# Optimization experiments

Hardware: AMD Instinct MI355X
Metric: run time of the kernel (lower is better)

## Reference

```python
import jax, jax.numpy as jnp
import numpy as np

S, B, D = 2048, 2, 1024
NH, DH, DI = 16, 64, 4096


def setup_inputs() -> dict:
    key = jax.random.key(0)
    ks = jax.random.split(key, 12)
    init_qkv = 1.0 / np.sqrt(D)
    init_out = 1.0 / np.sqrt(NH * DH)
    stdm = 1.0 / np.sqrt(D)
    stdi = 1.0 / np.sqrt(DI)

    def u(k, shape, lo, hi):
        return jax.random.uniform(k, shape, jnp.float32, lo, hi)

    inp = {}
    inp["dec_inp"] = jax.random.normal(ks[0], (S, B, D), jnp.float32)
    # causal mask: True = masked (future key j > query i); shape [q, k, batch]
    causal = jnp.triu(jnp.ones((S, S), bool), k=1)
    inp["attn_mask"] = jnp.broadcast_to(causal[:, :, None], (S, S, B))
    inp["query_mean"] = u(ks[1], (NH * DH, D), -init_qkv, init_qkv)
    inp["key_mean"] = u(ks[2], (NH * DH, D), -init_qkv, init_qkv)
    inp["value_mean"] = u(ks[3], (NH * DH, D), -init_qkv, init_qkv)
    inp["query_std"] = u(ks[4], (NH * DH, D), 2 * np.log(init_qkv), np.log(init_qkv))
    inp["key_std"] = u(ks[5], (NH * DH, D), 2 * np.log(init_qkv), np.log(init_qkv))
    inp["value_std"] = u(ks[6], (NH * DH, D), 2 * np.log(init_qkv), np.log(init_qkv))
    inp["output_mean"] = u(ks[7], (D, NH * DH), -init_out, init_out)
    inp["output_std"] = u(ks[8], (D, NH * DH), 2 * np.log(init_out), np.log(init_out))
    inp["ln1_gamma"] = jnp.ones((D,), jnp.float32)
    inp["ln1_beta"] = jnp.zeros((D,), jnp.float32)
    inp["w1_mean"] = u(ks[9], (DI, D), -stdm, stdm)
    inp["w2_mean"] = u(ks[10], (D, DI), -stdi, stdi)
    inp["w1_std"] = u(ks[11], (DI, D), 2 * np.log(stdm), np.log(stdm))
    inp["w2_std"] = u(jax.random.fold_in(key, 99), (D, DI), 2 * np.log(stdi), np.log(stdi))
    inp["ln2_gamma"] = jnp.ones((D,), jnp.float32)
    inp["ln2_beta"] = jnp.zeros((D,), jnp.float32)
    return inp


def _layer_norm(x, g, b, eps=1e-5):
    mu = jnp.mean(x, -1, keepdims=True)
    var = jnp.mean((x - mu) ** 2, -1, keepdims=True)
    return g * (x - mu) * jax.lax.rsqrt(var + eps) + b


def _kl(theta_mean, theta_std):
    return jnp.mean(theta_mean ** 2 - 2.0 * theta_std + jnp.exp(2.0 * theta_std)) / 2.0


def reference(dec_inp, attn_mask, query_mean, key_mean, value_mean, query_std,
              key_std, value_std, output_mean, output_std, ln1_gamma, ln1_beta,
              w1_mean, w2_mean, w1_std, w2_std, ln2_gamma, ln2_beta):
    scale = 1.0 / (DH ** 0.5)
    # QKV projections (eval mode: no Bayesian weight sampling, diffs are 0)
    head_q = jnp.einsum('ibd,hd->ibh', dec_inp, query_mean).reshape(S, B, NH, DH)
    head_k = jnp.einsum('ibd,hd->ibh', dec_inp, key_mean).reshape(S, B, NH, DH)
    head_v = jnp.einsum('ibd,hd->ibh', dec_inp, value_mean).reshape(S, B, NH, DH)
    attn_score = jnp.einsum('ibnd,jbnd->ijbn', head_q, head_k) * scale
    attn_score = jnp.where(attn_mask[:, :, :, None], -jnp.inf, attn_score)
    attn_prob = jax.nn.softmax(attn_score, axis=1)  # softmax over key dim j
    attn_vec = jnp.einsum('ijbn,jbnd->ibnd', attn_prob, head_v).reshape(S, B, NH * DH)
    # NOTE: the original code (bug-faithfully) projects with value_mean, not output_mean
    attn_out = jnp.einsum('ibh,dh->ibd', attn_vec, value_mean)
    h = _layer_norm(dec_inp + attn_out, ln1_gamma, ln1_beta)
    attn_kl = _kl(
        jnp.concatenate([query_mean, key_mean, value_mean, output_mean.T], -1),
        jnp.concatenate([query_std, key_std, value_std, output_std.T], -1))
    # Bayesian positionwise FF (no activation in BayesPositionwiseFF)
    l1 = jnp.einsum('ibd,fd->ibf', h, w1_mean)
    l2 = jnp.einsum('ibf,df->ibd', l1, w2_mean)
    out = _layer_norm(h + l2, ln2_gamma, ln2_beta)
    ff_kl = _kl(jnp.concatenate([w1_mean, w2_mean.T], -1),
                jnp.concatenate([w1_std, w2_std.T], -1))
    return out, attn_kl + ff_kl
```

## Files before the change

kernel.cpp:

```cpp
#include <hip/hip_runtime.h>

#define S_LEN  2048
#define BATCH  2
#define DMODEL 1024
#define NHEADS 16
#define DHEAD  64
#define DFF    4096
#define MROWS  (S_LEN*BATCH)
#define QKVN   3072

typedef __attribute__((ext_vector_type(8))) short bf16x8;
typedef __attribute__((ext_vector_type(4))) float f32x4;
typedef __attribute__((ext_vector_type(4))) short s16x4;

#define NEG_BIG (-3.0e38f)
#define SCALE_LOG2 (0.125f * 1.4426950408889634f)

__device__ __forceinline__ short f2bf(float f){
  unsigned u = __float_as_uint(f);
  u += 0x7fffu + ((u >> 16) & 1u);
  return (short)(u >> 16);
}

__device__ __forceinline__ void gload16(const void* gptr, void* lptr){
  __builtin_amdgcn_global_load_lds(
      (const __attribute__((address_space(1))) unsigned int*)gptr,
      (__attribute__((address_space(3))) unsigned int*)lptr,
      16, 0, 0);
}

__global__ __launch_bounds__(256) void cast_kernel(const float* __restrict__ in,
                                                   short* __restrict__ out, int n){
  int i = (blockIdx.x * 256 + threadIdx.x) * 4;
  if (i >= n) return;
  f32x4 v = *(const f32x4*)(in + i);
  s16x4 o;
  o[0] = f2bf(v[0]); o[1] = f2bf(v[1]); o[2] = f2bf(v[2]); o[3] = f2bf(v[3]);
  *(s16x4*)(out + i) = o;
}

template<int BN>
__global__ __launch_bounds__(512) void gemm_bt(const short* __restrict__ A,
                                               const short* __restrict__ Bt,
                                               float* __restrict__ Cf,
                                               short* __restrict__ Cb,
                                               int M, int N, int K){
  __shared__ short As[128][32];
  __shared__ short Bs[BN][32];
  constexpr int NB = BN / 32;
  const int t = threadIdx.x;
  const int lane = t & 63, w = t >> 6;
  const int m0 = blockIdx.y * 128, n0 = blockIdx.x * BN;
  const int wm = (w & 3) * 32, wn = (w >> 2) * (BN / 2);
  const int lr = lane & 15, lg = lane >> 4;

  f32x4 acc[2][NB] = {};

  const short* Ap = A  + (size_t)(m0 + (t >> 2)) * K + (t & 3) * 8;
  const short* Bp = Bt + (size_t)(n0 + ((t & (BN * 4 - 1)) >> 2)) * K + (t & 3) * 8;
  char* ldsA = (char*)(&As[0][0]) + w * 1024;
  char* ldsB = (char*)(&Bs[0][0]) + (w & (BN / 32 * 2 - 1)) * 1024;

  for (int k0 = 0; k0 < K; k0 += 32){
    gload16(Ap + k0, ldsA);
    if (BN == 128 || t < 256) gload16(Bp + k0, ldsB);
    __syncthreads();
    bf16x8 a0 = *(const bf16x8*)&As[wm      + lr][lg * 8];
    bf16x8 a1 = *(const bf16x8*)&As[wm + 16 + lr][lg * 8];
    bf16x8 bfr[NB];
    for (int ni = 0; ni < NB; ni++)
      bfr[ni] = *(const bf16x8*)&Bs[wn + ni * 16 + lr][lg * 8];
    for (int ni = 0; ni < NB; ni++){
      acc[0][ni] = __builtin_amdgcn_mfma_f32_16x16x32_bf16(a0, bfr[ni], acc[0][ni], 0, 0, 0);
      acc[1][ni] = __builtin_amdgcn_mfma_f32_16x16x32_bf16(a1, bfr[ni], acc[1][ni], 0, 0, 0);
    }
    __syncthreads();
  }

  for (int mi = 0; mi < 2; mi++){
    for (int ni = 0; ni < NB; ni++){
      int row = m0 + wm + mi * 16 + lg * 4;
      int col = n0 + wn + ni * 16 + lr;
      for (int r = 0; r < 4; r++){
        float v = acc[mi][ni][r];
        if (Cf) Cf[(size_t)(row + r) * N + col] = v;
        if (Cb) Cb[(size_t)(row + r) * N + col] = f2bf(v);
      }
    }
  }
}

__global__ __launch_bounds__(256) void attn_kernel(const short* __restrict__ QKV,
                                                   short* __restrict__ AV){
  __shared__ short Ks[64][64];
  __shared__ short Vst[64][64];
  __shared__ short Pt[4][16][64];
  const int t = threadIdx.x, lane = t & 63, w = t >> 6;
  const int hb = blockIdx.y;
  const int b = hb >> 4, n = hb & 15;
  const int lr = lane & 15, lg = lane >> 4;

  for (int half = 0; half < 2; half++){
    const int qt = half ? (31 - (int)blockIdx.x) : (int)blockIdx.x;
    const int q0w = qt * 64 + w * 16;

    bf16x8 aq[2];
    {
      const short* qp = QKV + ((size_t)(q0w + lr) * BATCH + b) * QKVN + n * DHEAD + lg * 8;
      aq[0] = *(const bf16x8*)(qp);
      aq[1] = *(const bf16x8*)(qp + 32);
    }

    f32x4 acc[4] = {};
    float m_run = NEG_BIG, l_run = 0.f;

    for (int jt = 0; jt <= qt; jt++){
      const int j0 = jt * 64;
      __syncthreads();
      {
        int j = t >> 2, u0 = (t & 3) * 2;
        const short* kp = QKV + ((size_t)(j0 + j) * BATCH + b) * QKVN + DMODEL + n * DHEAD + u0 * 8;
        *(bf16x8*)&Ks[j][(u0 ^ (j & 7)) * 8]       = *(const bf16x8*)(kp);
        *(bf16x8*)&Ks[j][((u0 + 1) ^ (j & 7)) * 8] = *(const bf16x8*)(kp + 8);
        int jv = t & 63, dq = (t >> 6) * 16;
        const short* vp = QKV + ((size_t)(j0 + jv) * BATCH + b) * QKVN + 2 * DMODEL + n * DHEAD + dq;
        bf16x8 v0 = *(const bf16x8*)(vp);
        bf16x8 v1 = *(const bf16x8*)(vp + 8);
        int uj = jv >> 3, jl = jv & 7;
        for (int e = 0; e < 8; e++){
          int sc = (((uj ^ e) << 3) | jl);
          Vst[dq + e][sc]     = v0[e];
          Vst[dq + 8 + e][sc] = v1[e];
        }
      }
      __syncthreads();

      f32x4 s[4];
      __builtin_amdgcn_s_setprio(1);
      for (int nf = 0; nf < 4; nf++){
        f32x4 z = {};
        for (int kk = 0; kk < 2; kk++){
          bf16x8 bk = *(const bf16x8*)&Ks[nf * 16 + lr][((kk * 4 + lg) ^ (lr & 7)) * 8];
          z = __builtin_amdgcn_mfma_f32_16x16x32_bf16(bk, aq[kk], z, 0, 0, 0);
        }
        s[nf] = z;
      }
      __builtin_amdgcn_s_setprio(0);

      for (int nf = 0; nf < 4; nf++)
        for (int r = 0; r < 4; r++) s[nf][r] *= SCALE_LOG2;

      if (jt == qt){
        int qg = q0w + lr;
        for (int nf = 0; nf < 4; nf++)
          for (int r = 0; r < 4; r++)
            if (j0 + nf * 16 + lg * 4 + r > qg) s[nf][r] = NEG_BIG;
      }

      float mx = NEG_BIG;
      for (int nf = 0; nf < 4; nf++){
        float a0 = fmaxf(s[nf][0], s[nf][1]);
        float a1 = fmaxf(s[nf][2], s[nf][3]);
        mx = fmaxf(mx, fmaxf(a0, a1));
      }
      mx = fmaxf(mx, __shfl_xor(mx, 16, 64));
      mx = fmaxf(mx, __shfl_xor(mx, 32, 64));
      float mn = fmaxf(m_run, mx);
      float corr = __builtin_exp2f(m_run - mn);
      m_run = mn;

      float rs = 0.f;
      for (int nf = 0; nf < 4; nf++)
        for (int r = 0; r < 4; r++){
          float p = __builtin_exp2f(s[nf][r] - mn);
          s[nf][r] = p;
          rs += p;
        }
      rs += __shfl_xor(rs, 16, 64);
      rs += __shfl_xor(rs, 32, 64);
      l_run = l_run * corr + rs;

      char* prow = (char*)&Pt[w][lr][0];
      for (int nf = 0; nf < 4; nf++){
        unsigned u0 = __float_as_uint(s[nf][0]);
        unsigned u1 = __float_as_uint(s[nf][1]);
        unsigned u2 = __float_as_uint(s[nf][2]);
        unsigned u3 = __float_as_uint(s[nf][3]);
        uint2 val;
        val.x = (u0 >> 16) | (u1 & 0xffff0000u);
        val.y = (u2 >> 16) | (u3 & 0xffff0000u);
        int off = ((((nf * 2) + (lg >> 1)) ^ (lr & 7)) << 4) + ((lg & 1) << 3);
        *(uint2*)(prow + off) = val;
      }

      float cb[4];
      for (int r = 0; r < 4; r++) cb[r] = __shfl(corr, lg * 4 + r, 64);
      for (int df = 0; df < 4; df++)
        for (int r = 0; r < 4; r++) acc[df][r] *= cb[r];

      __builtin_amdgcn_s_setprio(1);
      for (int kk = 0; kk < 2; kk++){
        bf16x8 pa = *(const bf16x8*)(prow + ((((kk * 4) + lg) ^ (lr & 7)) << 4));
        for (int df = 0; df < 4; df++){
          bf16x8 bv = *(const bf16x8*)&Vst[df * 16 + lr][((kk * 4 + lg) ^ (lr & 7)) * 8];
          acc[df] = __builtin_amdgcn_mfma_f32_16x16x32_bf16(pa, bv, acc[df], 0, 0, 0);
        }
      }
      __builtin_amdgcn_s_setprio(0);
    }

    float lb[4];
    for (int r = 0; r < 4; r++) lb[r] = __shfl(l_run, lg * 4 + r, 64);
    for (int df = 0; df < 4; df++){
      for (int r = 0; r < 4; r++){
        int i_glob = q0w + lg * 4 + r;
        AV[((size_t)i_glob * BATCH + b) * DMODEL + n * DHEAD + df * 16 + lr] =
            f2bf(acc[df][r] / lb[r]);
      }
    }
    __syncthreads();
  }
}

__global__ __launch_bounds__(256) void ln_kernel(const float* __restrict__ xa,
                                                 const float* __restrict__ xb,
                                                 const float* __restrict__ gamma,
                                                 const float* __restrict__ beta,
                                                 float* __restrict__ outF,
                                                 short* __restrict__ outB){
  __shared__ float red[4];
  const int row = blockIdx.x, t = threadIdx.x;
  const size_t base = (size_t)row * DMODEL + t * 4;
  f32x4 a  = *(const f32x4*)(xa + base);
  f32x4 bb = *(const f32x4*)(xb + base);
  f32x4 x;
  for (int e = 0; e < 4; e++) x[e] = a[e] + bb[e];
  float sum = x[0] + x[1] + x[2] + x[3];
  for (int m = 1; m < 64; m <<= 1) sum += __shfl_xor(sum, m, 64);
  if ((t & 63) == 0) red[t >> 6] = sum;
  __syncthreads();
  float mu = (red[0] + red[1] + red[2] + red[3]) * (1.f / DMODEL);
  float sq = 0.f;
  for (int e = 0; e < 4; e++){ float d = x[e] - mu; sq += d * d; }
  for (int m = 1; m < 64; m <<= 1) sq += __shfl_xor(sq, m, 64);
  __syncthreads();
  if ((t & 63) == 0) red[t >> 6] = sq;
  __syncthreads();
  float var = (red[0] + red[1] + red[2] + red[3]) * (1.f / DMODEL);
  float rstd = rsqrtf(var + 1e-5f);
  f32x4 g  = *(const f32x4*)(gamma + t * 4);
  f32x4 be = *(const f32x4*)(beta + t * 4);
  for (int e = 0; e < 4; e++){
    float y = g[e] * (x[e] - mu) * rstd + be[e];
    if (outF) outF[base + e] = y;
    if (outB) outB[base + e] = f2bf(y);
  }
}

__global__ __launch_bounds__(256) void kl_kernel(const float* __restrict__ mean,
                                                 const float* __restrict__ stdv,
                                                 int n, double* acc){
  __shared__ double red[4];
  double local = 0.0;
  int stride = gridDim.x * 256;
  for (int i = blockIdx.x * 256 + threadIdx.x; i < n; i += stride){
    float m = mean[i], s = stdv[i];
    local += (double)(m * m) - 2.0 * (double)s + (double)expf(2.f * s);
  }
  for (int msk = 1; msk < 64; msk <<= 1) local += __shfl_xor(local, msk, 64);
  const int t = threadIdx.x;
  if ((t & 63) == 0) red[t >> 6] = local;
  __syncthreads();
  if (t == 0) atomicAdd(acc, red[0] + red[1] + red[2] + red[3]);
}

__global__ void kl_final(const double* acc, float* out){
  out[0] = (float)(acc[0] / 8388608.0 + acc[1] / 16777216.0);
}

extern "C" void kernel_launch(void* const* d_in, const int* in_sizes, int n_in,
                              void* d_out, int out_size, void* d_ws, size_t ws_size,
                              hipStream_t stream){
  (void)in_sizes; (void)n_in; (void)out_size; (void)ws_size;
  const float* dec = (const float*)d_in[0];
  const float* qm  = (const float*)d_in[2];
  const float* km  = (const float*)d_in[3];
  const float* vm  = (const float*)d_in[4];
  const float* qs  = (const float*)d_in[5];
  const float* ks  = (const float*)d_in[6];
  const float* vs  = (const float*)d_in[7];
  const float* om  = (const float*)d_in[8];
  const float* os_ = (const float*)d_in[9];
  const float* g1  = (const float*)d_in[10];
  const float* b1  = (const float*)d_in[11];
  const float* w1m = (const float*)d_in[12];
  const float* w2m = (const float*)d_in[13];
  const float* w1s = (const float*)d_in[14];
  const float* w2s = (const float*)d_in[15];
  const float* g2  = (const float*)d_in[16];
  const float* b2  = (const float*)d_in[17];
  float* out = (float*)d_out;

  char* ws = (char*)d_ws;
  size_t off = 0;
  auto alloc = [&](size_t bytes) -> char* {
    char* p = ws + off;
    off += (bytes + 255) & ~(size_t)255;
    return p;
  };
  short* Xb   = (short*)alloc((size_t)MROWS * DMODEL * 2);
  short* Wqkv = (short*)alloc((size_t)QKVN * DMODEL * 2);
  short* W1   = (short*)alloc((size_t)DFF * DMODEL * 2);
  short* W2   = (short*)alloc((size_t)DMODEL * DFF * 2);
  short* Wv   = Wqkv + (size_t)2 * DMODEL * DMODEL;
  short* QKVb = (short*)alloc((size_t)MROWS * QKVN * 2);
  short* AVb  = (short*)alloc((size_t)MROWS * DMODEL * 2);
  float* tmpF = (float*)alloc((size_t)MROWS * DMODEL * 4);
  float* hF   = (float*)alloc((size_t)MROWS * DMODEL * 4);
  double* acc = (double*)alloc(256);
  short* L1 = QKVb;

  hipMemsetAsync(acc, 0, 16, stream);

  cast_kernel<<<MROWS * DMODEL / 1024, 256, 0, stream>>>(dec, Xb, MROWS * DMODEL);
  cast_kernel<<<DMODEL * DMODEL / 1024, 256, 0, stream>>>(qm, Wqkv, DMODEL * DMODEL);
  cast_kernel<<<DMODEL * DMODEL / 1024, 256, 0, stream>>>(km, Wqkv + (size_t)DMODEL * DMODEL, DMODEL * DMODEL);
  cast_kernel<<<DMODEL * DMODEL / 1024, 256, 0, stream>>>(vm, Wqkv + (size_t)2 * DMODEL * DMODEL, DMODEL * DMODEL);
  cast_kernel<<<DFF * DMODEL / 1024, 256, 0, stream>>>(w1m, W1, DFF * DMODEL);
  cast_kernel<<<DMODEL * DFF / 1024, 256, 0, stream>>>(w2m, W2, DMODEL * DFF);

  gemm_bt<128><<<dim3(QKVN / 128, MROWS / 128), 512, 0, stream>>>(Xb, Wqkv, nullptr, QKVb, MROWS, QKVN, DMODEL);

  attn_kernel<<<dim3(16, BATCH * NHEADS), 256, 0, stream>>>(QKVb, AVb);

  gemm_bt<64><<<dim3(DMODEL / 64, MROWS / 128), 512, 0, stream>>>(AVb, Wv, tmpF, nullptr, MROWS, DMODEL, DMODEL);

  ln_kernel<<<MROWS, 256, 0, stream>>>(dec, tmpF, g1, b1, hF, Xb);

  gemm_bt<128><<<dim3(DFF / 128, MROWS / 128), 512, 0, stream>>>(Xb, W1, nullptr, L1, MROWS, DFF, DMODEL);
  gemm_bt<64><<<dim3(DMODEL / 64, MROWS / 128), 512, 0, stream>>>(L1, W2, tmpF, nullptr, MROWS, DMODEL, DFF);

  ln_kernel<<<MROWS, 256, 0, stream>>>(hF, tmpF, g2, b2, out, nullptr);

  kl_kernel<<<1024, 256, 0, stream>>>(qm, qs, DMODEL * DMODEL, acc);
  kl_kernel<<<1024, 256, 0, stream>>>(km, ks, DMODEL * DMODEL, acc);
  kl_kernel<<<1024, 256, 0, stream>>>(vm, vs, DMODEL * DMODEL, acc);
  kl_kernel<<<1024, 256, 0, stream>>>(om, os_, DMODEL * DMODEL, acc);
  kl_kernel<<<1024, 256, 0, stream>>>(w1m, w1s, DFF * DMODEL, acc + 1);
  kl_kernel<<<1024, 256, 0, stream>>>(w2m, w2s, DMODEL * DFF, acc + 1);
  kl_final<<<1, 1, 0, stream>>>(acc, out + (size_t)MROWS * DMODEL);
}
```

Before: 542.3 us.

## Double-buffer GEMM LDS tiles, remap blocks across XCDs, fuse weight cast with KL

The GEMM now keeps two LDS buffers and issues the global-to-LDS load of the next K tile before computing on the current one, with one barrier per iteration instead of two. This lets memory latency overlap with MFMA work. Blocks are launched on a 1D grid and remapped so consecutive IDs go round-robin over the 8 XCDs, which aims to improve L2 locality. The weight bf16 casts are also fused with the KL reductions, so the mean weights are read once rather than twice, and the six separate KL launches go away.

```diff
diff --git a/kernel.cpp b/kernel.cpp
--- a/kernel.cpp
+++ b/kernel.cpp
@@ -39,18 +39,50 @@
   *(s16x4*)(out + i) = o;
 }
 
+__global__ __launch_bounds__(256) void cast_kl_kernel(const float* __restrict__ mean,
+                                                      const float* __restrict__ stdv,
+                                                      short* __restrict__ outb,
+                                                      int n, double* acc){
+  __shared__ double red[4];
+  double local = 0.0;
+  const int stride = gridDim.x * 1024;
+  for (int i = (blockIdx.x * 256 + threadIdx.x) * 4; i < n; i += stride){
+    f32x4 m = *(const f32x4*)(mean + i);
+    f32x4 sv = *(const f32x4*)(stdv + i);
+    if (outb){
+      s16x4 o;
+      o[0] = f2bf(m[0]); o[1] = f2bf(m[1]); o[2] = f2bf(m[2]); o[3] = f2bf(m[3]);
+      *(s16x4*)(outb + i) = o;
+    }
+    for (int e = 0; e < 4; e++)
+      local += (double)(m[e] * m[e]) - 2.0 * (double)sv[e] + (double)expf(2.f * sv[e]);
+  }
+  for (int msk = 1; msk < 64; msk <<= 1) local += __shfl_xor(local, msk, 64);
+  const int t = threadIdx.x;
+  if ((t & 63) == 0) red[t >> 6] = local;
+  __syncthreads();
+  if (t == 0) atomicAdd(acc, red[0] + red[1] + red[2] + red[3]);
+}
+
+__global__ void kl_final(const double* acc, float* out){
+  out[0] = (float)(acc[0] / 8388608.0 + acc[1] / 16777216.0);
+}
+
 template<int BN>
 __global__ __launch_bounds__(512) void gemm_bt(const short* __restrict__ A,
                                                const short* __restrict__ Bt,
                                                float* __restrict__ Cf,
                                                short* __restrict__ Cb,
-                                               int M, int N, int K){
-  __shared__ short As[128][32];
-  __shared__ short Bs[BN][32];
+                                               int M, int N, int K, int nbx){
+  __shared__ short As[2][128][32];
+  __shared__ short Bs[2][BN][32];
   constexpr int NB = BN / 32;
   const int t = threadIdx.x;
   const int lane = t & 63, w = t >> 6;
-  const int m0 = blockIdx.y * 128, n0 = blockIdx.x * BN;
+  const int q8 = (int)gridDim.x >> 3;
+  const int sid = ((int)blockIdx.x & 7) * q8 + ((int)blockIdx.x >> 3);
+  const int bx = sid % nbx, by = sid / nbx;
+  const int m0 = by * 128, n0 = bx * BN;
   const int wm = (w & 3) * 32, wn = (w >> 2) * (BN / 2);
   const int lr = lane & 15, lg = lane >> 4;
 
@@ -58,23 +90,35 @@
 
   const short* Ap = A  + (size_t)(m0 + (t >> 2)) * K + (t & 3) * 8;
   const short* Bp = Bt + (size_t)(n0 + ((t & (BN * 4 - 1)) >> 2)) * K + (t & 3) * 8;
-  char* ldsA = (char*)(&As[0][0]) + w * 1024;
-  char* ldsB = (char*)(&Bs[0][0]) + (w & (BN / 32 * 2 - 1)) * 1024;
-
+  char* ldsA0 = (char*)As + w * 1024;
+  char* ldsB0 = (char*)Bs + (w & (NB * 2 - 1)) * 1024;
+  constexpr int BSTRIDE = BN * 64;
+
+  gload16(Ap, ldsA0);
+  if (BN == 128 || t < 256) gload16(Bp, ldsB0);
+  asm volatile("s_waitcnt vmcnt(0)" ::: "memory");
+  __builtin_amdgcn_s_barrier();
+  asm volatile("" ::: "memory");
+
+  int cur = 0;
   for (int k0 = 0; k0 < K; k0 += 32){
-    gload16(Ap + k0, ldsA);
-    if (BN == 128 || t < 256) gload16(Bp + k0, ldsB);
-    __syncthreads();
-    bf16x8 a0 = *(const bf16x8*)&As[wm      + lr][lg * 8];
-    bf16x8 a1 = *(const bf16x8*)&As[wm + 16 + lr][lg * 8];
+    if (k0 + 32 < K){
+      gload16(Ap + k0 + 32, ldsA0 + (cur ^ 1) * 8192);
+      if (BN == 128 || t < 256) gload16(Bp + k0 + 32, ldsB0 + (cur ^ 1) * BSTRIDE);
+    }
+    bf16x8 a0 = *(const bf16x8*)&As[cur][wm      + lr][lg * 8];
+    bf16x8 a1 = *(const bf16x8*)&As[cur][wm + 16 + lr][lg * 8];
     bf16x8 bfr[NB];
     for (int ni = 0; ni < NB; ni++)
-      bfr[ni] = *(const bf16x8*)&Bs[wn + ni * 16 + lr][lg * 8];
+      bfr[ni] = *(const bf16x8*)&Bs[cur][wn + ni * 16 + lr][lg * 8];
     for (int ni = 0; ni < NB; ni++){
       acc[0][ni] = __builtin_amdgcn_mfma_f32_16x16x32_bf16(a0, bfr[ni], acc[0][ni], 0, 0, 0);
       acc[1][ni] = __builtin_amdgcn_mfma_f32_16x16x32_bf16(a1, bfr[ni], acc[1][ni], 0, 0, 0);
     }
-    __syncthreads();
+    asm volatile("s_waitcnt vmcnt(0)" ::: "memory");
+    __builtin_amdgcn_s_barrier();
+    asm volatile("" ::: "memory");
+    cur ^= 1;
   }
 
   for (int mi = 0; mi < 2; mi++){
@@ -257,27 +301,6 @@
   }
 }
 
-__global__ __launch_bounds__(256) void kl_kernel(const float* __restrict__ mean,
-                                                 const float* __restrict__ stdv,
-                                                 int n, double* acc){
-  __shared__ double red[4];
-  double local = 0.0;
-  int stride = gridDim.x * 256;
-  for (int i = blockIdx.x * 256 + threadIdx.x; i < n; i += stride){
-    float m = mean[i], s = stdv[i];
-    local += (double)(m * m) - 2.0 * (double)s + (double)expf(2.f * s);
-  }
-  for (int msk = 1; msk < 64; msk <<= 1) local += __shfl_xor(local, msk, 64);
-  const int t = threadIdx.x;
-  if ((t & 63) == 0) red[t >> 6] = local;
-  __syncthreads();
-  if (t == 0) atomicAdd(acc, red[0] + red[1] + red[2] + red[3]);
-}
-
-__global__ void kl_final(const double* acc, float* out){
-  out[0] = (float)(acc[0] / 8388608.0 + acc[1] / 16777216.0);
-}
-
 extern "C" void kernel_launch(void* const* d_in, const int* in_sizes, int n_in,
                               void* d_out, int out_size, void* d_ws, size_t ws_size,
                               hipStream_t stream){
@@ -323,30 +346,25 @@
   hipMemsetAsync(acc, 0, 16, stream);
 
   cast_kernel<<<MROWS * DMODEL / 1024, 256, 0, stream>>>(dec, Xb, MROWS * DMODEL);
-  cast_kernel<<<DMODEL * DMODEL / 1024, 256, 0, stream>>>(qm, Wqkv, DMODEL * DMODEL);
-  cast_kernel<<<DMODEL * DMODEL / 1024, 256, 0, stream>>>(km, Wqkv + (size_t)DMODEL * DMODEL, DMODEL * DMODEL);
-  cast_kernel<<<DMODEL * DMODEL / 1024, 256, 0, stream>>>(vm, Wqkv + (size_t)2 * DMODEL * DMODEL, DMODEL * DMODEL);
-  cast_kernel<<<DFF * DMODEL / 1024, 256, 0, stream>>>(w1m, W1, DFF * DMODEL);
-  cast_kernel<<<DMODEL * DFF / 1024, 256, 0, stream>>>(w2m, W2, DMODEL * DFF);
-
-  gemm_bt<128><<<dim3(QKVN / 128, MROWS / 128), 512, 0, stream>>>(Xb, Wqkv, nullptr, QKVb, MROWS, QKVN, DMODEL);
+  cast_kl_kernel<<<1024, 256, 0, stream>>>(qm, qs, Wqkv, DMODEL * DMODEL, acc);
+  cast_kl_kernel<<<1024, 256, 0, stream>>>(km, ks, Wqkv + (size_t)DMODEL * DMODEL, DMODEL * DMODEL, acc);
+  cast_kl_kernel<<<1024, 256, 0, stream>>>(vm, vs, Wqkv + (size_t)2 * DMODEL * DMODEL, DMODEL * DMODEL, acc);
+  cast_kl_kernel<<<1024, 256, 0, stream>>>(om, os_, nullptr, DMODEL * DMODEL, acc);
+  cast_kl_kernel<<<1024, 256, 0, stream>>>(w1m, w1s, W1, DFF * DMODEL, acc + 1);
+  cast_kl_kernel<<<1024, 256, 0, stream>>>(w2m, w2s, W2, DMODEL * DFF, acc + 1);
+
+  gemm_bt<128><<<(QKVN / 128) * (MROWS / 128), 512, 0, stream>>>(Xb, Wqkv, nullptr, QKVb, MROWS, QKVN, DMODEL, QKVN / 128);
 
   attn_kernel<<<dim3(16, BATCH * NHEADS), 256, 0, stream>>>(QKVb, AVb);
 
-  gemm_bt<64><<<dim3(DMODEL / 64, MROWS / 128), 512, 0, stream>>>(AVb, Wv, tmpF, nullptr, MROWS, DMODEL, DMODEL);
+  gemm_bt<64><<<(DMODEL / 64) * (MROWS / 128), 512, 0, stream>>>(AVb, Wv, tmpF, nullptr, MROWS, DMODEL, DMODEL, DMODEL / 64);
 
   ln_kernel<<<MROWS, 256, 0, stream>>>(dec, tmpF, g1, b1, hF, Xb);
 
-  gemm_bt<128><<<dim3(DFF / 128, MROWS / 128), 512, 0, stream>>>(Xb, W1, nullptr, L1, MROWS, DFF, DMODEL);
-  gemm_bt<64><<<dim3(DMODEL / 64, MROWS / 128), 512, 0, stream>>>(L1, W2, tmpF, nullptr, MROWS, DMODEL, DFF);
+  gemm_bt<128><<<(DFF / 128) * (MROWS / 128), 512, 0, stream>>>(Xb, W1, nullptr, L1, MROWS, DFF, DMODEL, DFF / 128);
+  gemm_bt<64><<<(DMODEL / 64) * (MROWS / 128), 512, 0, stream>>>(L1, W2, tmpF, nullptr, MROWS, DMODEL, DFF, DMODEL / 64);
 
   ln_kernel<<<MROWS, 256, 0, stream>>>(hF, tmpF, g2, b2, out, nullptr);
 
-  kl_kernel<<<1024, 256, 0, stream>>>(qm, qs, DMODEL * DMODEL, acc);
-  kl_kernel<<<1024, 256, 0, stream>>>(km, ks, DMODEL * DMODEL, acc);
-  kl_kernel<<<1024, 256, 0, stream>>>(vm, vs, DMODEL * DMODEL, acc);
-  kl_kernel<<<1024, 256, 0, stream>>>(om, os_, DMODEL * DMODEL, acc);
-  kl_kernel<<<1024, 256, 0, stream>>>(w1m, w1s, DFF * DMODEL, acc + 1);
-  kl_kernel<<<1024, 256, 0, stream>>>(w2m, w2s, DMODEL * DFF, acc + 1);
   kl_final<<<1, 1, 0, stream>>>(acc, out + (size_t)MROWS * DMODEL);
 }
```

After: 523.4 us. 3.5% less time.
